# Performance work log

Measured on AMD Instinct MI355X. Metric: run time of the kernel, lower is better.

Reference implementation:

```python
import jax, jax.numpy as jnp
import numpy as np

DN = ('NCHW', 'OIHW', 'NCHW')

def _conv(x, w, groups=1, padding=0):
    return jax.lax.conv_general_dilated(
        x, w, window_strides=(1, 1), padding=[(padding, padding)] * 2,
        dimension_numbers=DN, feature_group_count=groups)

def _bn(x, scale, shift):
    # precomputed inference BN: x * scale + shift, per channel (NCHW)
    return x * scale[None, :, None, None] + shift[None, :, None, None]

def _channel_shuffle(x, g):
    n, c, h, w = x.shape
    return x.reshape(n, g, c // g, h, w).transpose(0, 2, 1, 3, 4).reshape(n, c, h, w)

def setup_inputs() -> dict:
    key = jax.random.key(0)
    ks = jax.random.split(key, 13)
    N, Cin, H, W = 32, 240, 56, 56
    Cout, G = 480, 3
    mid = Cout // 4  # 120
    inp = {
        'x': jax.random.normal(ks[0], (N, Cin, H, W), jnp.float32),
        'w1': jax.random.normal(ks[1], (mid, Cin // G, 1, 1), jnp.float32) * 0.05,
        'scale1': jax.random.uniform(ks[2], (mid,), jnp.float32, 0.5, 1.5),
        'shift1': jax.random.normal(ks[3], (mid,), jnp.float32) * 0.1,
        'w2': jax.random.normal(ks[4], (mid, 1, 3, 3), jnp.float32) * 0.05,
        'scale2': jax.random.uniform(ks[5], (mid,), jnp.float32, 0.5, 1.5),
        'shift2': jax.random.normal(ks[6], (mid,), jnp.float32) * 0.1,
        'w3': jax.random.normal(ks[7], (Cout, mid // G, 1, 1), jnp.float32) * 0.05,
        'scale3': jax.random.uniform(ks[8], (Cout,), jnp.float32, 0.5, 1.5),
        'shift3': jax.random.normal(ks[9], (Cout,), jnp.float32) * 0.1,
        'wsc': jax.random.normal(ks[10], (Cout, Cin, 1, 1), jnp.float32) * 0.05,
        'scale_sc': jax.random.uniform(ks[11], (Cout,), jnp.float32, 0.5, 1.5),
        'shift_sc': jax.random.normal(ks[12], (Cout,), jnp.float32) * 0.1,
        'groups': G,
    }
    return inp

def reference(x, w1, scale1, shift1, w2, scale2, shift2, w3, scale3, shift3,
              wsc, scale_sc, shift_sc, groups):
    g = int(groups)
    mid = w1.shape[0]
    # conv1 (grouped 1x1) -> fused BN + ReLU
    y = _conv(x, w1, groups=g)
    y = jax.nn.relu(_bn(y, scale1, shift1))
    # conv2 (depthwise 3x3) -> fused BN + channel shuffle
    y = _conv(y, w2, groups=mid, padding=1)
    y = _channel_shuffle(_bn(y, scale2, shift2), g)
    # conv3 (grouped 1x1)
    y = _conv(y, w3, groups=g)
    # shortcut: 1x1 conv (in_channels != out_channels)
    z = _conv(x, wsc)
    # fused final: relu(BN3(y)) + BN_sc(z)
    return jax.nn.relu(_bn(y, scale3, shift3)) + _bn(z, scale_sc, shift_sc)
```

## Files before the change

### kernel.cpp

```cpp
#include <hip/hip_runtime.h>

typedef short bf16x8 __attribute__((ext_vector_type(8)));
typedef float f32x4 __attribute__((ext_vector_type(4)));

namespace {
constexpr int kHW = 3136;
constexpr int kNPx = 32 * kHW;
constexpr int kPtiles = kNPx / 16;
constexpr size_t kXbiShorts = (size_t)kPtiles * 4096;
constexpr size_t kY2iShorts = (size_t)kPtiles * 2048;
}

__device__ __align__(16) unsigned short g_w1i[3 * 4 * 48 * 32];
__device__ __align__(16) unsigned short g_wsci[8 * 480 * 32];
__device__ __align__(16) unsigned short g_w3i[2 * 480 * 32];
__device__ __align__(16) float g_w2f[9 * 120];

static __device__ __forceinline__ unsigned short f2b(float f) {
  unsigned u = __float_as_uint(f);
  u = (u + 0x7fffu + ((u >> 16) & 1u)) >> 16;
  return (unsigned short)u;
}
static __device__ __forceinline__ float b2f(unsigned short u) {
  return __uint_as_float((unsigned)u << 16);
}
static __device__ __forceinline__ f32x4 mfma16(bf16x8 a, bf16x8 b, f32x4 c) {
  return __builtin_amdgcn_mfma_f32_16x16x32_bf16(a, b, c, 0, 0, 0);
}
static __device__ __forceinline__ bf16x8 ldg8(const unsigned short* p) {
  return *reinterpret_cast<const bf16x8*>(p);
}

__global__ __launch_bounds__(256) void prep_weights(
    const float* __restrict__ w1, const float* __restrict__ wsc,
    const float* __restrict__ w3, const float* __restrict__ w2,
    const float* __restrict__ scale2) {
  const int idx = blockIdx.x * 256 + threadIdx.x;
  if (idx < 18432) {
    const int g = idx / 6144, r = idx % 6144, kb = r / 1536;
    const int j = (r % 1536) / 32, k = r % 32;
    const int gk = g * 64 + kb * 32 + k;
    const int c = gk - g * 80;
    unsigned short v = 0;
    if (j < 40 && c >= 0 && c < 80) v = f2b(w1[(g * 40 + j) * 80 + c]);
    g_w1i[idx] = v;
  } else if (idx < 18432 + 122880) {
    const int i = idx - 18432;
    const int kb = i / 15360, co = (i % 15360) / 32, k = i % 32;
    const int c = kb * 32 + k;
    g_wsci[i] = (c < 240) ? f2b(wsc[co * 240 + c]) : (unsigned short)0;
  } else if (idx < 18432 + 122880 + 30720) {
    const int i = idx - 141312;
    const int kb = i / 15360, co = (i % 15360) / 32, k = i % 32;
    const int cb = co / 160;
    const int s = cb * 32 + kb * 32 + k - cb * 40;
    g_w3i[i] = (s >= 0 && s < 40) ? f2b(w3[co * 40 + s]) : (unsigned short)0;
  } else if (idx < 18432 + 122880 + 30720 + 1080) {
    const int i = idx - 172032;
    const int tap = i / 120, c = i % 120;
    g_w2f[i] = w2[c * 9 + tap] * scale2[c];
  }
}

__global__ __launch_bounds__(256) void transpose_interleave(
    const float* __restrict__ x, unsigned short* __restrict__ xbi) {
  const int P0 = blockIdx.x * 64;
  const int px_loc = threadIdx.x >> 2, part = threadIdx.x & 3;
  const int P = P0 + px_loc;
  const int n = P / kHW, hw = P % kHW;
  const int pt = px_loc >> 4, l = px_loc & 15;
  unsigned short* dst =
      xbi + ((size_t)(P0 / 16) + pt) * 4096 + l * 32 + part * 8;
  const float* xp = x + ((size_t)n * 240) * kHW + hw;
#pragma unroll
  for (int kb = 0; kb < 8; ++kb) {
    unsigned short v[8];
#pragma unroll
    for (int j = 0; j < 8; ++j) {
      const int c = kb * 32 + part * 8 + j;
      v[j] = (c < 240) ? f2b(xp[(size_t)c * kHW]) : (unsigned short)0;
    }
    *reinterpret_cast<uint4*>(dst + kb * 512) =
        *reinterpret_cast<const uint4*>(v);
  }
}

__global__ __launch_bounds__(256) void conv1_gemm(
    const unsigned short* __restrict__ xbi, const float* __restrict__ scale1,
    const float* __restrict__ shift1, unsigned short* __restrict__ y1) {
  const int lane = threadIdx.x & 63;
  const int wv = threadIdx.x >> 6;
  const int l15 = lane & 15, quad = lane >> 4;
  const size_t PT = (size_t)blockIdx.x * 8 + wv * 2;

#pragma unroll
  for (int g = 0; g < 3; ++g) {
    f32x4 acc[2][3];
#pragma unroll
    for (int mt = 0; mt < 2; ++mt)
#pragma unroll
      for (int nt = 0; nt < 3; ++nt) acc[mt][nt] = (f32x4){0.f, 0.f, 0.f, 0.f};
#pragma unroll
    for (int kb = 0; kb < 4; ++kb) {
      const int kbi = 2 * g + kb;
      bf16x8 A[2];
#pragma unroll
      for (int mt = 0; mt < 2; ++mt)
        A[mt] = ldg8(xbi + (PT + mt) * 4096 + kbi * 512 + l15 * 32 + quad * 8);
#pragma unroll
      for (int nt = 0; nt < 3; ++nt) {
        const bf16x8 B = ldg8(g_w1i + (((g * 4 + kb) * 48) + nt * 16 + l15) * 32 +
                              quad * 8);
#pragma unroll
        for (int mt = 0; mt < 2; ++mt) acc[mt][nt] = mfma16(A[mt], B, acc[mt][nt]);
      }
    }
#pragma unroll
    for (int nt = 0; nt < 3; ++nt) {
      const int j = nt * 16 + l15;
      if (j < 40) {
        const int c = g * 40 + j;
        const float sc = scale1[c], sh = shift1[c];
#pragma unroll
        for (int mt = 0; mt < 2; ++mt) {
          const size_t pxb = (PT + mt) * 16 + quad * 4;
#pragma unroll
          for (int r = 0; r < 4; ++r) {
            float v = fmaf(acc[mt][nt][r], sc, sh);
            v = v > 0.f ? v : 0.f;
            y1[(pxb + r) * 120 + c] = f2b(v);
          }
        }
      }
    }
  }
}

__global__ __launch_bounds__(256) void dw_shuffle(
    const unsigned short* __restrict__ y1, const float* __restrict__ shift2,
    unsigned short* __restrict__ y2i) {
  const int idx = blockIdx.x * 256 + threadIdx.x;
  const int px = idx / 15, m = idx % 15;
  const int c0 = m * 8;
  const int n = px / kHW, hw = px % kHW;
  const int h = hw / 56, w = hw % 56;

  float acc[8];
  {
    const float4 s0 = *reinterpret_cast<const float4*>(shift2 + c0);
    const float4 s1 = *reinterpret_cast<const float4*>(shift2 + c0 + 4);
    acc[0] = s0.x; acc[1] = s0.y; acc[2] = s0.z; acc[3] = s0.w;
    acc[4] = s1.x; acc[5] = s1.y; acc[6] = s1.z; acc[7] = s1.w;
  }
  const unsigned short* yb = y1 + (size_t)n * kHW * 120 + c0;
#pragma unroll
  for (int dy = 0; dy < 3; ++dy) {
    const int hh = h + dy - 1;
    if (hh < 0 || hh >= 56) continue;
#pragma unroll
    for (int dx = 0; dx < 3; ++dx) {
      const int ww = w + dx - 1;
      if (ww < 0 || ww >= 56) continue;
      const bf16x8 v = ldg8(yb + (size_t)(hh * 56 + ww) * 120);
      const float* wp = g_w2f + (dy * 3 + dx) * 120 + c0;
      float wv_[8];
      *reinterpret_cast<float4*>(wv_) = *reinterpret_cast<const float4*>(wp);
      *reinterpret_cast<float4*>(wv_ + 4) =
          *reinterpret_cast<const float4*>(wp + 4);
#pragma unroll
      for (int j = 0; j < 8; ++j)
        acc[j] = fmaf(b2f((unsigned short)v[j]), wv_[j], acc[j]);
    }
  }
  const size_t base = ((size_t)(px >> 4)) * 2048 + (px & 15) * 32;
#pragma unroll
  for (int j = 0; j < 8; ++j) {
    const int c = c0 + j;
    const int cn = (c % 40) * 3 + c / 40;
    y2i[base + (cn >> 5) * 512 + (cn & 31)] = f2b(acc[j]);
  }
}

__global__ __launch_bounds__(256, 3) void conv3_sc_gemm(
    const unsigned short* __restrict__ xbi,
    const unsigned short* __restrict__ y2i, const float* __restrict__ scale3,
    const float* __restrict__ shift3, const float* __restrict__ ssc,
    const float* __restrict__ bsc, float* __restrict__ out) {
  const int pxb = blockIdx.x % 784;
  const int cb = blockIdx.x / 784;
  const int P0 = pxb * 128;
  const int lane = threadIdx.x & 63;
  const int wv = threadIdx.x >> 6;
  const int mh = wv & 1, nh = wv >> 1;
  const int l15 = lane & 15, quad = lane >> 4;
  const int cbase = cb * 160 + nh * 80;

  f32x4 acc[4][5];
#pragma unroll
  for (int mt = 0; mt < 4; ++mt)
#pragma unroll
    for (int nt = 0; nt < 5; ++nt) acc[mt][nt] = (f32x4){0.f, 0.f, 0.f, 0.f};

  const size_t PT = (size_t)(P0 / 16) + mh * 4;

#pragma unroll
  for (int kb = 0; kb < 2; ++kb) {
    const int kbi = cb + kb;
    bf16x8 A[4];
#pragma unroll
    for (int mt = 0; mt < 4; ++mt)
      A[mt] = ldg8(y2i + (PT + mt) * 2048 + kbi * 512 + l15 * 32 + quad * 8);
#pragma unroll
    for (int nt = 0; nt < 5; ++nt) {
      const bf16x8 B =
          ldg8(g_w3i + ((kb * 480) + cbase + nt * 16 + l15) * 32 + quad * 8);
#pragma unroll
      for (int mt = 0; mt < 4; ++mt) acc[mt][nt] = mfma16(A[mt], B, acc[mt][nt]);
    }
  }

#pragma unroll
  for (int nt = 0; nt < 5; ++nt) {
    const int co = cbase + nt * 16 + l15;
    const float s3 = scale3[co], h3 = shift3[co];
    const float is = 1.0f / ssc[co], h_ = bsc[co];
#pragma unroll
    for (int mt = 0; mt < 4; ++mt)
#pragma unroll
      for (int r = 0; r < 4; ++r) {
        float v3 = fmaf(acc[mt][nt][r], s3, h3);
        v3 = v3 > 0.f ? v3 : 0.f;
        acc[mt][nt][r] = (v3 + h_) * is;
      }
  }

  for (int kb = 0; kb < 8; ++kb) {
    bf16x8 A[4];
#pragma unroll
    for (int mt = 0; mt < 4; ++mt)
      A[mt] = ldg8(xbi + (PT + mt) * 4096 + kb * 512 + l15 * 32 + quad * 8);
#pragma unroll
    for (int nt = 0; nt < 5; ++nt) {
      const bf16x8 B =
          ldg8(g_wsci + ((kb * 480) + cbase + nt * 16 + l15) * 32 + quad * 8);
#pragma unroll
      for (int mt = 0; mt < 4; ++mt) acc[mt][nt] = mfma16(A[mt], B, acc[mt][nt]);
    }
  }

#pragma unroll
  for (int mt = 0; mt < 4; ++mt) {
    const int P = P0 + mh * 64 + mt * 16 + quad * 4;
    const int n = P / kHW, hw = P % kHW;
    float* ob = out + (size_t)n * 480 * kHW + hw;
#pragma unroll
    for (int nt = 0; nt < 5; ++nt) {
      const int co = cbase + nt * 16 + l15;
      const float s_ = ssc[co];
      float4 r;
      float* rp = reinterpret_cast<float*>(&r);
#pragma unroll
      for (int r4 = 0; r4 < 4; ++r4) rp[r4] = s_ * acc[mt][nt][r4];
      *reinterpret_cast<float4*>(ob + (size_t)co * kHW) = r;
    }
  }
}

extern "C" void kernel_launch(void* const* d_in, const int* in_sizes, int n_in,
                              void* d_out, int out_size, void* d_ws,
                              size_t ws_size, hipStream_t stream) {
  const float* x = (const float*)d_in[0];
  const float* w1 = (const float*)d_in[1];
  const float* scale1 = (const float*)d_in[2];
  const float* shift1 = (const float*)d_in[3];
  const float* w2 = (const float*)d_in[4];
  const float* scale2 = (const float*)d_in[5];
  const float* shift2 = (const float*)d_in[6];
  const float* w3 = (const float*)d_in[7];
  const float* scale3 = (const float*)d_in[8];
  const float* shift3 = (const float*)d_in[9];
  const float* wsc = (const float*)d_in[10];
  const float* ssc = (const float*)d_in[11];
  const float* bsc = (const float*)d_in[12];
  float* out = (float*)d_out;

  unsigned short* xbi = (unsigned short*)d_ws;
  unsigned short* y2i = xbi + kXbiShorts;
  unsigned short* y1 = y2i + kY2iShorts;

  prep_weights<<<677, 256, 0, stream>>>(w1, wsc, w3, w2, scale2);
  transpose_interleave<<<kNPx / 64, 256, 0, stream>>>(x, xbi);
  conv1_gemm<<<kPtiles / 8, 256, 0, stream>>>(xbi, scale1, shift1, y1);
  dw_shuffle<<<kNPx * 15 / 256, 256, 0, stream>>>(y1, shift2, y2i);
  conv3_sc_gemm<<<784 * 3, 256, 0, stream>>>(xbi, y2i, scale3, shift3, ssc,
                                             bsc, out);
}
```

Measured before the change: 461.8 us.

## Stage depthwise outputs in LDS for coalesced shuffle writes and remap conv3 blocks

The depthwise+shuffle kernel now handles one 16-pixel tile per block. It stages fp32 results in shared memory and then writes the shuffled, interleaved bf16 layout with one 16-byte vector store per thread, replacing scattered 2-byte stores. The zero padding for channels 120..127 is now written explicitly. Separately, the conv3/shortcut GEMM block index is remapped so the three channel blocks of a pixel tile are adjacent and spread across XCDs, aiming to improve L2 reuse of the shared xbi/y2i inputs. This costs a syncthreads, and 16 of the 256 threads sit idle during the compute phase.

```diff
diff --git a/kernel.cpp b/kernel.cpp
--- a/kernel.cpp
+++ b/kernel.cpp
@@ -139,46 +139,63 @@
 __global__ __launch_bounds__(256) void dw_shuffle(
     const unsigned short* __restrict__ y1, const float* __restrict__ shift2,
     unsigned short* __restrict__ y2i) {
-  const int idx = blockIdx.x * 256 + threadIdx.x;
-  const int px = idx / 15, m = idx % 15;
-  const int c0 = m * 8;
-  const int n = px / kHW, hw = px % kHW;
-  const int h = hw / 56, w = hw % 56;
-
-  float acc[8];
-  {
-    const float4 s0 = *reinterpret_cast<const float4*>(shift2 + c0);
-    const float4 s1 = *reinterpret_cast<const float4*>(shift2 + c0 + 4);
-    acc[0] = s0.x; acc[1] = s0.y; acc[2] = s0.z; acc[3] = s0.w;
-    acc[4] = s1.x; acc[5] = s1.y; acc[6] = s1.z; acc[7] = s1.w;
-  }
-  const unsigned short* yb = y1 + (size_t)n * kHW * 120 + c0;
-#pragma unroll
-  for (int dy = 0; dy < 3; ++dy) {
-    const int hh = h + dy - 1;
-    if (hh < 0 || hh >= 56) continue;
-#pragma unroll
-    for (int dx = 0; dx < 3; ++dx) {
-      const int ww = w + dx - 1;
-      if (ww < 0 || ww >= 56) continue;
-      const bf16x8 v = ldg8(yb + (size_t)(hh * 56 + ww) * 120);
-      const float* wp = g_w2f + (dy * 3 + dx) * 120 + c0;
-      float wv_[8];
-      *reinterpret_cast<float4*>(wv_) = *reinterpret_cast<const float4*>(wp);
-      *reinterpret_cast<float4*>(wv_ + 4) =
-          *reinterpret_cast<const float4*>(wp + 4);
-#pragma unroll
-      for (int j = 0; j < 8; ++j)
-        acc[j] = fmaf(b2f((unsigned short)v[j]), wv_[j], acc[j]);
-    }
-  }
-  const size_t base = ((size_t)(px >> 4)) * 2048 + (px & 15) * 32;
+  const int pt = blockIdx.x;
+  const int t = threadIdx.x;
+  __shared__ float lds_y2[16 * 121];
+
+  if (t < 240) {
+    const int px_l = t / 15, m = t % 15;
+    const int c0 = m * 8;
+    const int px = pt * 16 + px_l;
+    const int n = px / kHW, hw = px % kHW;
+    const int h = hw / 56, w = hw % 56;
+
+    float acc[8];
+    {
+      const float4 s0 = *reinterpret_cast<const float4*>(shift2 + c0);
+      const float4 s1 = *reinterpret_cast<const float4*>(shift2 + c0 + 4);
+      acc[0] = s0.x; acc[1] = s0.y; acc[2] = s0.z; acc[3] = s0.w;
+      acc[4] = s1.x; acc[5] = s1.y; acc[6] = s1.z; acc[7] = s1.w;
+    }
+    const unsigned short* yb = y1 + (size_t)n * kHW * 120 + c0;
+#pragma unroll
+    for (int dy = 0; dy < 3; ++dy) {
+      const int hh = h + dy - 1;
+      if (hh >= 0 && hh < 56) {
+#pragma unroll
+        for (int dx = 0; dx < 3; ++dx) {
+          const int ww = w + dx - 1;
+          if (ww >= 0 && ww < 56) {
+            const bf16x8 v = ldg8(yb + (size_t)(hh * 56 + ww) * 120);
+            const float* wp = g_w2f + (dy * 3 + dx) * 120 + c0;
+            float wv_[8];
+            *reinterpret_cast<float4*>(wv_) =
+                *reinterpret_cast<const float4*>(wp);
+            *reinterpret_cast<float4*>(wv_ + 4) =
+                *reinterpret_cast<const float4*>(wp + 4);
+#pragma unroll
+            for (int j = 0; j < 8; ++j)
+              acc[j] = fmaf(b2f((unsigned short)v[j]), wv_[j], acc[j]);
+          }
+        }
+      }
+    }
+#pragma unroll
+    for (int j = 0; j < 8; ++j) lds_y2[px_l * 121 + c0 + j] = acc[j];
+  }
+  __syncthreads();
+
+  const int q = t * 8;
+  const int kb = q >> 9, r = q & 511, pxl = r >> 5, k0 = r & 31;
+  unsigned short v[8];
 #pragma unroll
   for (int j = 0; j < 8; ++j) {
-    const int c = c0 + j;
-    const int cn = (c % 40) * 3 + c / 40;
-    y2i[base + (cn >> 5) * 512 + (cn & 31)] = f2b(acc[j]);
-  }
+    const int cn = kb * 32 + k0 + j;
+    const int c = (cn % 3) * 40 + cn / 3;
+    v[j] = (cn < 120) ? f2b(lds_y2[pxl * 121 + c]) : (unsigned short)0;
+  }
+  *reinterpret_cast<uint4*>(y2i + (size_t)pt * 2048 + q) =
+      *reinterpret_cast<const uint4*>(v);
 }
 
 __global__ __launch_bounds__(256, 3) void conv3_sc_gemm(
@@ -186,8 +203,10 @@
     const unsigned short* __restrict__ y2i, const float* __restrict__ scale3,
     const float* __restrict__ shift3, const float* __restrict__ ssc,
     const float* __restrict__ bsc, float* __restrict__ out) {
-  const int pxb = blockIdx.x % 784;
-  const int cb = blockIdx.x / 784;
+  const int bid = blockIdx.x;
+  const int l = (bid & 7) * 294 + (bid >> 3);
+  const int pxb = l / 3;
+  const int cb = l % 3;
   const int P0 = pxb * 128;
   const int lane = threadIdx.x & 63;
   const int wv = threadIdx.x >> 6;
@@ -291,7 +310,7 @@
   prep_weights<<<677, 256, 0, stream>>>(w1, wsc, w3, w2, scale2);
   transpose_interleave<<<kNPx / 64, 256, 0, stream>>>(x, xbi);
   conv1_gemm<<<kPtiles / 8, 256, 0, stream>>>(xbi, scale1, shift1, y1);
-  dw_shuffle<<<kNPx * 15 / 256, 256, 0, stream>>>(y1, shift2, y2i);
+  dw_shuffle<<<kPtiles, 256, 0, stream>>>(y1, shift2, y2i);
   conv3_sc_gemm<<<784 * 3, 256, 0, stream>>>(xbi, y2i, scale3, shift3, ssc,
                                              bsc, out);
 }
```

New measurement: 431.6 us. 1.07x faster.
